# Kernel tuning notes

Hardware: AMD Instinct MI355X
Metric: run time of the kernel (lower is better)

The kernel has to match this reference:

```python
import math
import jax
import jax.numpy as jnp
import numpy as np

SEGMENT_SIZE = 2048   # w (init: segment_size)
DILATION_RATE = 4     # r (init: dilation_rate)
D_MODEL = 1024        # init: d_model


def _sparse_indices(n: int, w: int, r: int, head_idx: int) -> np.ndarray:
    """Static SparsifyIndices: per segment of size w, take tokens offset::r.
    Since r divides w, every segment yields exactly m=w//r indices (no -1 pad).
    Returns flat global token indices, shape (S*m,)."""
    S = n // w
    m = w // r
    off = head_idx % r
    seg_start = np.arange(S, dtype=np.int64)[:, None] * w      # (S,1)
    within = off + r * np.arange(m, dtype=np.int64)[None, :]   # (1,m)
    return (seg_start + within).reshape(-1)


def setup_inputs() -> dict:
    key = jax.random.key(0)
    x = jax.random.normal(key, (4, 8192, D_MODEL), dtype=jnp.float32)
    return {"x": x, "head_idx": 1}


def reference(x, head_idx):
    b, n0, d = x.shape
    w, r = SEGMENT_SIZE, DILATION_RATE
    pad = (-n0) % w
    if pad:
        x = jnp.pad(x, ((0, 0), (0, pad), (0, 0)))
    n = n0 + pad
    idx = _sparse_indices(n, w, r, int(head_idx))  # static, (S*m,)
    S, m = n // w, w // r

    # Gather dilated tokens per segment: (b, S, m, d)
    xg = x[:, idx, :].reshape(b, S, m, d)

    # Softmax attention within each sub-segment (q=k=v=xg)
    scores = jnp.einsum('bsid,bsjd->bsij', xg, xg) / math.sqrt(d)  # (b,S,m,m)
    probs = jax.nn.softmax(scores, axis=-1)
    att = jnp.einsum('bsij,bsjd->bsid', probs, xg).reshape(b, S * m, d)

    # MixOutputs: alpha-weighted scatter-add back to full sequence
    denoms = att.sum(-1)                                       # (b, S*m)
    denom_sums = jnp.zeros((b, n), x.dtype).at[:, idx].add(denoms)
    alphas = denoms / denom_sums[:, idx]                       # (b, S*m)
    out = jnp.zeros((b, n, d), x.dtype).at[:, idx, :].add(att * alphas[..., None])
    return out
```

## Files before the change

### kernel.cpp

```cpp
#include <hip/hip_runtime.h>
#include <hip/hip_bf16.h>


typedef __bf16 bf16_t;
typedef __bf16 bf16x8 __attribute__((ext_vector_type(8)));
typedef float floatx4 __attribute__((ext_vector_type(4)));

#define D_MODEL 1024
#define SEG_W   2048
#define RATE    4
#define M_SUB   512
#define NTOK    8192
#define NSEGT   16
#define XG_ELEMS ((long)NSEGT * M_SUB * D_MODEL)

__device__ __forceinline__ void gload16(const bf16_t* g, bf16_t* l) {
    __builtin_amdgcn_global_load_lds(
        (const __attribute__((address_space(1))) void*)g,
        (__attribute__((address_space(3))) void*)l, 16, 0, 0);
}

#define MFMA16(a, b, c) __builtin_amdgcn_mfma_f32_16x16x32_bf16((a), (b), (c), 0, 0, 0)

__global__ __launch_bounds__(256) void gather_kernel(
    const float* __restrict__ x, const int* __restrict__ hidp,
    bf16_t* __restrict__ xg, bf16_t* __restrict__ xgT)
{
    const int off = ((hidp[0] % RATE) + RATE) % RATE;
    const int bid = blockIdx.x;
    const int seg = bid >> 7;
    const int rem = bid & 127;
    const int it  = rem >> 4;
    const int dt  = rem & 15;
    const int b   = seg >> 2, s = seg & 3;

    __shared__ ushort tile[64][65];

    const int t  = threadIdx.x;
    const int r  = t >> 2;
    const int cq = (t & 3) << 4;

    union U8 { bf16x8 v; ushort u[8]; };

    {
        const int  i   = it * 64 + r;
        const long tok = (long)s * SEG_W + off + 4L * i;
        const float* src = x + ((long)b * NTOK + tok) * D_MODEL + dt * 64 + cq;
        float4 f0 = ((const float4*)src)[0];
        float4 f1 = ((const float4*)src)[1];
        float4 f2 = ((const float4*)src)[2];
        float4 f3 = ((const float4*)src)[3];
        U8 lo, hi;
        lo.v[0]=(bf16_t)f0.x; lo.v[1]=(bf16_t)f0.y; lo.v[2]=(bf16_t)f0.z; lo.v[3]=(bf16_t)f0.w;
        lo.v[4]=(bf16_t)f1.x; lo.v[5]=(bf16_t)f1.y; lo.v[6]=(bf16_t)f1.z; lo.v[7]=(bf16_t)f1.w;
        hi.v[0]=(bf16_t)f2.x; hi.v[1]=(bf16_t)f2.y; hi.v[2]=(bf16_t)f2.z; hi.v[3]=(bf16_t)f2.w;
        hi.v[4]=(bf16_t)f3.x; hi.v[5]=(bf16_t)f3.y; hi.v[6]=(bf16_t)f3.z; hi.v[7]=(bf16_t)f3.w;
        bf16_t* dstg = xg + ((long)seg * M_SUB + i) * D_MODEL + dt * 64 + cq;
        *(bf16x8*)(dstg)     = lo.v;
        *(bf16x8*)(dstg + 8) = hi.v;
        #pragma unroll
        for (int j = 0; j < 8; ++j) { tile[r][cq + j] = lo.u[j]; tile[r][cq + 8 + j] = hi.u[j]; }
    }
    __syncthreads();
    {
        const int dc = r;
        const int iq = cq;
        U8 o0, o1;
        #pragma unroll
        for (int j = 0; j < 8; ++j) { o0.u[j] = tile[iq + j][dc]; o1.u[j] = tile[iq + 8 + j][dc]; }
        bf16_t* dstT = xgT + ((long)seg * D_MODEL + dt * 64 + dc) * M_SUB + it * 64 + iq;
        *(bf16x8*)(dstT)     = o0.v;
        *(bf16x8*)(dstT + 8) = o1.v;
    }
}

__global__ __launch_bounds__(512, 2) void attn_kernel(
    const bf16_t* __restrict__ xg, const bf16_t* __restrict__ xgT,
    const int* __restrict__ hidp, float* __restrict__ out)
{
    const int off  = ((hidp[0] % RATE) + RATE) % RATE;
    const int bid0 = blockIdx.x;
    const int sub  = bid0 >> 3;
    const int seg  = (bid0 & 7) * 2 + (sub >> 4);
    const int band = sub & 15;
    const int b = seg >> 2, s = seg & 3;

    const int tid  = threadIdx.x;
    const int w    = tid >> 6;
    const int lane = tid & 63;
    const int l16  = lane & 15;
    const int quad = lane >> 4;

    __shared__ alignas(16) char arena[133120];
    bf16_t* Kring = (bf16_t*)arena;
    float (*redmax)[32] = (float(*)[32])(arena + 131072);
    float (*redsum)[32] = (float(*)[32])(arena + 132096);
    bf16_t* Pl    = (bf16_t*)arena;
    bf16_t* Vring = (bf16_t*)(arena + 32768);

    const bf16_t* xs = xg + (long)seg * M_SUB * D_MODEL;

    const bf16_t* qr0 = xs + (long)(band * 32 + l16) * D_MODEL + quad * 8;
    const bf16_t* qr1 = qr0 + 16 * D_MODEL;

    const bf16_t* ksrc = xs + (long)(w * 64 + (lane >> 2)) * D_MODEL
                            + (((lane & 3) ^ (lane >> 4)) * 8);
    auto stageK = [&](int buf, int t) {
        bf16_t* dst = Kring + buf * 16384 + (w * 64) * 32;
        const bf16_t* src = ksrc + t * 32;
        #pragma unroll
        for (int j = 0; j < 4; ++j)
            gload16(src + j * 16 * D_MODEL, dst + j * 512);
    };

    const bf16_t* vsrc = xgT + ((long)seg * D_MODEL + w * 64 + (lane >> 2)) * M_SUB
                             + (((lane & 3) ^ (lane >> 4)) * 8);
    auto stageV = [&](int buf, int p, int t) {
        bf16_t* dst = Vring + buf * 16384 + (w * 64) * 32;
        const bf16_t* src = vsrc + (long)p * 512 * M_SUB + t * 32;
        #pragma unroll
        for (int j = 0; j < 4; ++j)
            gload16(src + j * 16 * M_SUB, dst + j * 512);
    };

    const int rsw = (l16 >> 2) & 3;

    floatx4 accS[2][4];
    #pragma unroll
    for (int m = 0; m < 2; ++m)
        #pragma unroll
        for (int n = 0; n < 4; ++n) accS[m][n] = (floatx4){0.f, 0.f, 0.f, 0.f};

    bf16x8 qf[4][2];
    #pragma unroll
    for (int p0 = 0; p0 < 3; ++p0) {
        qf[p0][0] = *(const bf16x8*)(qr0 + p0 * 32);
        qf[p0][1] = *(const bf16x8*)(qr1 + p0 * 32);
        stageK(p0, p0);
    }

    #pragma unroll
    for (int t = 0; t < 32; ++t) {
        if (t <= 29)      asm volatile("s_waitcnt vmcnt(12)" ::: "memory");
        else if (t == 30) asm volatile("s_waitcnt vmcnt(6)"  ::: "memory");
        else              asm volatile("s_waitcnt vmcnt(0)"  ::: "memory");

        const bf16_t* Kb = Kring + (t & 3) * 16384;
        bf16x8 Bf[4];
        #pragma unroll
        for (int n = 0; n < 4; ++n) {
            const int row = w * 64 + n * 16 + l16;
            Bf[n] = *(const bf16x8*)&Kb[row * 32 + ((quad ^ rsw) * 8)];
        }
        if (t <= 28) {
            qf[(t + 3) & 3][0] = *(const bf16x8*)(qr0 + (t + 3) * 32);
            qf[(t + 3) & 3][1] = *(const bf16x8*)(qr1 + (t + 3) * 32);
            stageK((t + 3) & 3, t + 3);
        }
        #pragma unroll
        for (int n = 0; n < 4; ++n) {
            accS[0][n] = MFMA16(qf[t & 3][0], Bf[n], accS[0][n]);
            accS[1][n] = MFMA16(qf[t & 3][1], Bf[n], accS[1][n]);
        }
    }

    #pragma unroll
    for (int m = 0; m < 2; ++m)
        #pragma unroll
        for (int n = 0; n < 4; ++n)
            #pragma unroll
            for (int rg = 0; rg < 4; ++rg) accS[m][n][rg] *= 0.03125f;

    float mx[2][4];
    #pragma unroll
    for (int m = 0; m < 2; ++m)
        #pragma unroll
        for (int rg = 0; rg < 4; ++rg)
            mx[m][rg] = fmaxf(fmaxf(accS[m][0][rg], accS[m][1][rg]),
                              fmaxf(accS[m][2][rg], accS[m][3][rg]));
    #pragma unroll
    for (int d = 1; d < 16; d <<= 1)
        #pragma unroll
        for (int m = 0; m < 2; ++m)
            #pragma unroll
            for (int rg = 0; rg < 4; ++rg)
                mx[m][rg] = fmaxf(mx[m][rg], __shfl_xor(mx[m][rg], d, 64));
    if (l16 == 0) {
        #pragma unroll
        for (int m = 0; m < 2; ++m)
            #pragma unroll
            for (int rg = 0; rg < 4; ++rg)
                redmax[w][m * 16 + quad * 4 + rg] = mx[m][rg];
    }
    __syncthreads();
    float gm[2][4];
    #pragma unroll
    for (int m = 0; m < 2; ++m)
        #pragma unroll
        for (int rg = 0; rg < 4; ++rg) {
            const int row = m * 16 + quad * 4 + rg;
            float g = redmax[0][row];
            #pragma unroll
            for (int ww = 1; ww < 8; ++ww) g = fmaxf(g, redmax[ww][row]);
            gm[m][rg] = g;
        }
    float sm[2][4] = {{0.f,0.f,0.f,0.f},{0.f,0.f,0.f,0.f}};
    #pragma unroll
    for (int m = 0; m < 2; ++m)
        #pragma unroll
        for (int n = 0; n < 4; ++n)
            #pragma unroll
            for (int rg = 0; rg < 4; ++rg) {
                const float e = __expf(accS[m][n][rg] - gm[m][rg]);
                accS[m][n][rg] = e;
                sm[m][rg] += e;
            }
    #pragma unroll
    for (int d = 1; d < 16; d <<= 1)
        #pragma unroll
        for (int m = 0; m < 2; ++m)
            #pragma unroll
            for (int rg = 0; rg < 4; ++rg)
                sm[m][rg] += __shfl_xor(sm[m][rg], d, 64);
    if (l16 == 0) {
        #pragma unroll
        for (int m = 0; m < 2; ++m)
            #pragma unroll
            for (int rg = 0; rg < 4; ++rg)
                redsum[w][m * 16 + quad * 4 + rg] = sm[m][rg];
    }
    __syncthreads();
    float iv[2][4];
    #pragma unroll
    for (int m = 0; m < 2; ++m)
        #pragma unroll
        for (int rg = 0; rg < 4; ++rg) {
            const int row = m * 16 + quad * 4 + rg;
            float tt = redsum[0][row];
            #pragma unroll
            for (int ww = 1; ww < 8; ++ww) tt += redsum[ww][row];
            iv[m][rg] = 1.f / tt;
        }

    stageV(0, 0, 0); stageV(1, 0, 1); stageV(2, 0, 2);

    #pragma unroll
    for (int m = 0; m < 2; ++m)
        #pragma unroll
        for (int rg = 0; rg < 4; ++rg) {
            const int row = m * 16 + quad * 4 + rg;
            const float f = iv[m][rg];
            #pragma unroll
            for (int n = 0; n < 4; ++n) {
                const int col = w * 64 + n * 16 + l16;
                const int sw  = (((col >> 3) ^ (row & 7)) << 3) + (col & 7);
                Pl[row * 512 + sw] = (bf16_t)(accS[m][n][rg] * f);
            }
        }
    asm volatile("s_waitcnt lgkmcnt(0)" ::: "memory");
    __builtin_amdgcn_s_barrier();
    __builtin_amdgcn_sched_barrier(0);

    floatx4 accA[2][4], accB[2][4];
    #pragma unroll
    for (int m = 0; m < 2; ++m)
        #pragma unroll
        for (int n = 0; n < 4; ++n) {
            accA[m][n] = (floatx4){0.f, 0.f, 0.f, 0.f};
            accB[m][n] = (floatx4){0.f, 0.f, 0.f, 0.f};
        }

    auto pv_pass = [&](int p, floatx4 (&acc)[2][4]) {
        #pragma unroll
        for (int t = 0; t < 16; ++t) {
            if (t <= 13)      asm volatile("s_waitcnt vmcnt(8)" ::: "memory");
            else if (t == 14) asm volatile("s_waitcnt vmcnt(4)" ::: "memory");
            else              asm volatile("s_waitcnt vmcnt(0)" ::: "memory");

            const bf16_t* Vb = Vring + (t % 3) * 16384;
            bf16x8 Af[2], Bf[4];
            const int ch = (t * 4 + quad) ^ (l16 & 7);
            #pragma unroll
            for (int m = 0; m < 2; ++m)
                Af[m] = *(const bf16x8*)&Pl[(m * 16 + l16) * 512 + ch * 8];
            #pragma unroll
            for (int n = 0; n < 4; ++n) {
                const int row = w * 64 + n * 16 + l16;
                Bf[n] = *(const bf16x8*)&Vb[row * 32 + ((quad ^ rsw) * 8)];
            }
            #pragma unroll
            for (int m = 0; m < 2; ++m)
                #pragma unroll
                for (int n = 0; n < 4; ++n)
                    acc[m][n] = MFMA16(Af[m], Bf[n], acc[m][n]);
            if (t <= 12) stageV(t % 3, p, t + 3);
        }
    };

    pv_pass(0, accA);
    stageV(0, 1, 0); stageV(1, 1, 1); stageV(2, 1, 2);
    pv_pass(1, accB);

    float* obase = out + (long)b * NTOK * D_MODEL;
    #pragma unroll
    for (int m = 0; m < 2; ++m)
        #pragma unroll
        for (int rg = 0; rg < 4; ++rg) {
            const long tok = (long)s * SEG_W + off + 4L * (band * 32 + m * 16 + quad * 4 + rg);
            float* orow = obase + tok * D_MODEL;
            #pragma unroll
            for (int n = 0; n < 4; ++n) {
                const int d = w * 64 + n * 16 + l16;
                __builtin_nontemporal_store(accA[m][n][rg], orow + d);
                __builtin_nontemporal_store(accB[m][n][rg], orow + 512 + d);
            }
        }

    {
        const floatx4 z = {0.f, 0.f, 0.f, 0.f};
        const int chunk = tid & 255;
        const int half  = tid >> 8;
        #pragma unroll 4
        for (int p = 0; p < 48; ++p) {
            const int t = p * 2 + half;
            const int q = t / 3, e = t % 3;
            const int delta = e + (e >= off ? 1 : 0);
            const long tok = (long)s * SEG_W + 4L * (band * 32 + q) + delta;
            __builtin_nontemporal_store(z, (floatx4*)(obase + tok * D_MODEL + chunk * 4));
        }
    }
}

extern "C" void kernel_launch(void* const* d_in, const int* in_sizes, int n_in,
                              void* d_out, int out_size, void* d_ws, size_t ws_size,
                              hipStream_t stream) {
    const float* x   = (const float*)d_in[0];
    const int*   hid = (const int*)d_in[1];
    float*       out = (float*)d_out;
    bf16_t* xg  = (bf16_t*)d_ws;
    bf16_t* xgT = xg + XG_ELEMS;

    gather_kernel<<<dim3(2048), dim3(256), 0, stream>>>(x, hid, xg, xgT);
    attn_kernel<<<dim3(256), dim3(512), 0, stream>>>(xg, xgT, hid, out);
}
```

Before: 253.4 us.

## Load K/V operands directly to registers and move zero-fill into gather kernel

Drops the LDS staging rings for K and V in the attention kernel. Each wave now loads its MFMA B operands straight from global memory into a 7-slot register ring, with counted vmcnt waits. The two PV passes are merged into one 32-step loop, and P fragments are double-buffered from LDS. The zero-fill of the non-selected output rows moves from the attention kernel's tail into the gather kernel, so it overlaps the gather work. The trade-off is much higher register pressure from the register rings and uncoalesced 16-byte row-strided global loads in place of cooperative LDS staging.

```diff
diff --git a/kernel.cpp b/kernel.cpp
--- a/kernel.cpp
+++ b/kernel.cpp
@@ -14,17 +14,28 @@
 #define NSEGT   16
 #define XG_ELEMS ((long)NSEGT * M_SUB * D_MODEL)
 
-__device__ __forceinline__ void gload16(const bf16_t* g, bf16_t* l) {
-    __builtin_amdgcn_global_load_lds(
-        (const __attribute__((address_space(1))) void*)g,
-        (__attribute__((address_space(3))) void*)l, 16, 0, 0);
+#define MFMA16(a, b, c) __builtin_amdgcn_mfma_f32_16x16x32_bf16((a), (b), (c), 0, 0, 0)
+
+__device__ __forceinline__ void vwait(int n) {
+    switch (n) {
+    case 0:  asm volatile("s_waitcnt vmcnt(0)"  ::: "memory"); break;
+    case 4:  asm volatile("s_waitcnt vmcnt(4)"  ::: "memory"); break;
+    case 6:  asm volatile("s_waitcnt vmcnt(6)"  ::: "memory"); break;
+    case 8:  asm volatile("s_waitcnt vmcnt(8)"  ::: "memory"); break;
+    case 12: asm volatile("s_waitcnt vmcnt(12)" ::: "memory"); break;
+    case 16: asm volatile("s_waitcnt vmcnt(16)" ::: "memory"); break;
+    case 18: asm volatile("s_waitcnt vmcnt(18)" ::: "memory"); break;
+    case 20: asm volatile("s_waitcnt vmcnt(20)" ::: "memory"); break;
+    case 24: asm volatile("s_waitcnt vmcnt(24)" ::: "memory"); break;
+    case 30: asm volatile("s_waitcnt vmcnt(30)" ::: "memory"); break;
+    case 36: asm volatile("s_waitcnt vmcnt(36)" ::: "memory"); break;
+    }
 }
-
-#define MFMA16(a, b, c) __builtin_amdgcn_mfma_f32_16x16x32_bf16((a), (b), (c), 0, 0, 0)
 
 __global__ __launch_bounds__(256) void gather_kernel(
     const float* __restrict__ x, const int* __restrict__ hidp,
-    bf16_t* __restrict__ xg, bf16_t* __restrict__ xgT)
+    bf16_t* __restrict__ xg, bf16_t* __restrict__ xgT,
+    float* __restrict__ out)
 {
     const int off = ((hidp[0] % RATE) + RATE) % RATE;
     const int bid = blockIdx.x;
@@ -72,6 +83,22 @@
         *(bf16x8*)(dstT)     = o0.v;
         *(bf16x8*)(dstT + 8) = o1.v;
     }
+
+    {
+        const floatx4 z = {0.f, 0.f, 0.f, 0.f};
+        const int i2 = r;
+        const int c4 = t & 3;
+        float* obase = out + (long)b * NTOK * D_MODEL + dt * 64;
+        #pragma unroll
+        for (int e = 0; e < 3; ++e) {
+            const int delta = e + (e >= off ? 1 : 0);
+            const long tok = (long)s * SEG_W + 4L * (it * 64 + i2) + delta;
+            floatx4* dst = (floatx4*)(obase + tok * D_MODEL);
+            #pragma unroll
+            for (int c = 0; c < 4; ++c)
+                __builtin_nontemporal_store(z, dst + c4 + 4 * c);
+        }
+    }
 }
 
 __global__ __launch_bounds__(512, 2) void attn_kernel(
@@ -91,76 +118,49 @@
     const int l16  = lane & 15;
     const int quad = lane >> 4;
 
-    __shared__ alignas(16) char arena[133120];
-    bf16_t* Kring = (bf16_t*)arena;
-    float (*redmax)[32] = (float(*)[32])(arena + 131072);
-    float (*redsum)[32] = (float(*)[32])(arena + 132096);
-    bf16_t* Pl    = (bf16_t*)arena;
-    bf16_t* Vring = (bf16_t*)(arena + 32768);
+    __shared__ alignas(16) bf16_t Pl[32 * 512];
+    __shared__ float redmax[8][32];
+    __shared__ float redsum[8][32];
 
     const bf16_t* xs = xg + (long)seg * M_SUB * D_MODEL;
 
     const bf16_t* qr0 = xs + (long)(band * 32 + l16) * D_MODEL + quad * 8;
     const bf16_t* qr1 = qr0 + 16 * D_MODEL;
-
-    const bf16_t* ksrc = xs + (long)(w * 64 + (lane >> 2)) * D_MODEL
-                            + (((lane & 3) ^ (lane >> 4)) * 8);
-    auto stageK = [&](int buf, int t) {
-        bf16_t* dst = Kring + buf * 16384 + (w * 64) * 32;
-        const bf16_t* src = ksrc + t * 32;
-        #pragma unroll
-        for (int j = 0; j < 4; ++j)
-            gload16(src + j * 16 * D_MODEL, dst + j * 512);
+    const bf16_t* kb0 = xs + (long)(w * 64 + l16) * D_MODEL + quad * 8;
+    const bf16_t* kb1 = kb0 + 16 * D_MODEL;
+    const bf16_t* kb2 = kb0 + 32 * D_MODEL;
+    const bf16_t* kb3 = kb0 + 48 * D_MODEL;
+
+    floatx4 accS[2][4];
+    #pragma unroll
+    for (int m = 0; m < 2; ++m)
+        #pragma unroll
+        for (int n = 0; n < 4; ++n) accS[m][n] = (floatx4){0.f, 0.f, 0.f, 0.f};
+
+    bf16x8 qf[7][2], kf[7][4];
+    auto issueQK = [&](int slot, int tt) {
+        const int o = tt * 32;
+        qf[slot][0] = *(const bf16x8*)(qr0 + o);
+        qf[slot][1] = *(const bf16x8*)(qr1 + o);
+        kf[slot][0] = *(const bf16x8*)(kb0 + o);
+        kf[slot][1] = *(const bf16x8*)(kb1 + o);
+        kf[slot][2] = *(const bf16x8*)(kb2 + o);
+        kf[slot][3] = *(const bf16x8*)(kb3 + o);
     };
 
-    const bf16_t* vsrc = xgT + ((long)seg * D_MODEL + w * 64 + (lane >> 2)) * M_SUB
-                             + (((lane & 3) ^ (lane >> 4)) * 8);
-    auto stageV = [&](int buf, int p, int t) {
-        bf16_t* dst = Vring + buf * 16384 + (w * 64) * 32;
-        const bf16_t* src = vsrc + (long)p * 512 * M_SUB + t * 32;
-        #pragma unroll
-        for (int j = 0; j < 4; ++j)
-            gload16(src + j * 16 * M_SUB, dst + j * 512);
-    };
-
-    const int rsw = (l16 >> 2) & 3;
-
-    floatx4 accS[2][4];
-    #pragma unroll
-    for (int m = 0; m < 2; ++m)
-        #pragma unroll
-        for (int n = 0; n < 4; ++n) accS[m][n] = (floatx4){0.f, 0.f, 0.f, 0.f};
-
-    bf16x8 qf[4][2];
-    #pragma unroll
-    for (int p0 = 0; p0 < 3; ++p0) {
-        qf[p0][0] = *(const bf16x8*)(qr0 + p0 * 32);
-        qf[p0][1] = *(const bf16x8*)(qr1 + p0 * 32);
-        stageK(p0, p0);
-    }
+    #pragma unroll
+    for (int p = 0; p < 6; ++p) issueQK(p, p);
 
     #pragma unroll
     for (int t = 0; t < 32; ++t) {
-        if (t <= 29)      asm volatile("s_waitcnt vmcnt(12)" ::: "memory");
-        else if (t == 30) asm volatile("s_waitcnt vmcnt(6)"  ::: "memory");
-        else              asm volatile("s_waitcnt vmcnt(0)"  ::: "memory");
-
-        const bf16_t* Kb = Kring + (t & 3) * 16384;
-        bf16x8 Bf[4];
+        if (t + 6 < 32) issueQK((t + 6) % 7, t + 6);
+        const int ahead = (31 - t) < 6 ? (31 - t) : 6;
+        vwait(6 * ahead);
+        const int sl = t % 7;
         #pragma unroll
         for (int n = 0; n < 4; ++n) {
-            const int row = w * 64 + n * 16 + l16;
-            Bf[n] = *(const bf16x8*)&Kb[row * 32 + ((quad ^ rsw) * 8)];
-        }
-        if (t <= 28) {
-            qf[(t + 3) & 3][0] = *(const bf16x8*)(qr0 + (t + 3) * 32);
-            qf[(t + 3) & 3][1] = *(const bf16x8*)(qr1 + (t + 3) * 32);
-            stageK((t + 3) & 3, t + 3);
-        }
-        #pragma unroll
-        for (int n = 0; n < 4; ++n) {
-            accS[0][n] = MFMA16(qf[t & 3][0], Bf[n], accS[0][n]);
-            accS[1][n] = MFMA16(qf[t & 3][1], Bf[n], accS[1][n]);
+            accS[0][n] = MFMA16(qf[sl][0], kf[sl][n], accS[0][n]);
+            accS[1][n] = MFMA16(qf[sl][1], kf[sl][n], accS[1][n]);
         }
     }
 
@@ -242,7 +242,22 @@
             iv[m][rg] = 1.f / tt;
         }
 
-    stageV(0, 0, 0); stageV(1, 0, 1); stageV(2, 0, 2);
+    const bf16_t* vb0 = xgT + ((long)seg * D_MODEL + w * 64 + l16) * M_SUB + quad * 8;
+    const bf16_t* vb1 = vb0 + 16 * M_SUB;
+    const bf16_t* vb2 = vb0 + 32 * M_SUB;
+    const bf16_t* vb3 = vb0 + 48 * M_SUB;
+
+    bf16x8 vf[7][4];
+    auto issueV = [&](int slot, int t) {
+        const int tt = t & 15;
+        const long po = (long)(t >> 4) * 512 * M_SUB + tt * 32;
+        vf[slot][0] = *(const bf16x8*)(vb0 + po);
+        vf[slot][1] = *(const bf16x8*)(vb1 + po);
+        vf[slot][2] = *(const bf16x8*)(vb2 + po);
+        vf[slot][3] = *(const bf16x8*)(vb3 + po);
+    };
+    #pragma unroll
+    for (int p = 0; p < 6; ++p) issueV(p, p);
 
     #pragma unroll
     for (int m = 0; m < 2; ++m)
@@ -270,36 +285,36 @@
             accB[m][n] = (floatx4){0.f, 0.f, 0.f, 0.f};
         }
 
-    auto pv_pass = [&](int p, floatx4 (&acc)[2][4]) {
-        #pragma unroll
-        for (int t = 0; t < 16; ++t) {
-            if (t <= 13)      asm volatile("s_waitcnt vmcnt(8)" ::: "memory");
-            else if (t == 14) asm volatile("s_waitcnt vmcnt(4)" ::: "memory");
-            else              asm volatile("s_waitcnt vmcnt(0)" ::: "memory");
-
-            const bf16_t* Vb = Vring + (t % 3) * 16384;
-            bf16x8 Af[2], Bf[4];
-            const int ch = (t * 4 + quad) ^ (l16 & 7);
-            #pragma unroll
-            for (int m = 0; m < 2; ++m)
-                Af[m] = *(const bf16x8*)&Pl[(m * 16 + l16) * 512 + ch * 8];
+    bf16x8 pf[2][2];
+    auto loadP = [&](int slot, int t) {
+        const int tt = t & 15;
+        const int ch = (tt * 4 + quad) ^ (l16 & 7);
+        pf[slot][0] = *(const bf16x8*)&Pl[(l16) * 512 + ch * 8];
+        pf[slot][1] = *(const bf16x8*)&Pl[(16 + l16) * 512 + ch * 8];
+    };
+    loadP(0, 0);
+
+    #pragma unroll
+    for (int t = 0; t < 32; ++t) {
+        if (t + 6 < 32) issueV((t + 6) % 7, t + 6);
+        const int ahead = (31 - t) < 6 ? (31 - t) : 6;
+        vwait(4 * ahead);
+        if (t + 1 < 32) loadP((t + 1) & 1, t + 1);
+        const int sl = t % 7;
+        if (t < 16) {
             #pragma unroll
             for (int n = 0; n < 4; ++n) {
-                const int row = w * 64 + n * 16 + l16;
-                Bf[n] = *(const bf16x8*)&Vb[row * 32 + ((quad ^ rsw) * 8)];
-            }
-            #pragma unroll
-            for (int m = 0; m < 2; ++m)
-                #pragma unroll
-                for (int n = 0; n < 4; ++n)
-                    acc[m][n] = MFMA16(Af[m], Bf[n], acc[m][n]);
-            if (t <= 12) stageV(t % 3, p, t + 3);
-        }
-    };
-
-    pv_pass(0, accA);
-    stageV(0, 1, 0); stageV(1, 1, 1); stageV(2, 1, 2);
-    pv_pass(1, accB);
+                accA[0][n] = MFMA16(pf[t & 1][0], vf[sl][n], accA[0][n]);
+                accA[1][n] = MFMA16(pf[t & 1][1], vf[sl][n], accA[1][n]);
+            }
+        } else {
+            #pragma unroll
+            for (int n = 0; n < 4; ++n) {
+                accB[0][n] = MFMA16(pf[t & 1][0], vf[sl][n], accB[0][n]);
+                accB[1][n] = MFMA16(pf[t & 1][1], vf[sl][n], accB[1][n]);
+            }
+        }
+    }
 
     float* obase = out + (long)b * NTOK * D_MODEL;
     #pragma unroll
@@ -315,20 +330,6 @@
                 __builtin_nontemporal_store(accB[m][n][rg], orow + 512 + d);
             }
         }
-
-    {
-        const floatx4 z = {0.f, 0.f, 0.f, 0.f};
-        const int chunk = tid & 255;
-        const int half  = tid >> 8;
-        #pragma unroll 4
-        for (int p = 0; p < 48; ++p) {
-            const int t = p * 2 + half;
-            const int q = t / 3, e = t % 3;
-            const int delta = e + (e >= off ? 1 : 0);
-            const long tok = (long)s * SEG_W + 4L * (band * 32 + q) + delta;
-            __builtin_nontemporal_store(z, (floatx4*)(obase + tok * D_MODEL + chunk * 4));
-        }
-    }
 }
 
 extern "C" void kernel_launch(void* const* d_in, const int* in_sizes, int n_in,
@@ -340,6 +341,6 @@
     bf16_t* xg  = (bf16_t*)d_ws;
     bf16_t* xgT = xg + XG_ELEMS;
 
-    gather_kernel<<<dim3(2048), dim3(256), 0, stream>>>(x, hid, xg, xgT);
+    gather_kernel<<<dim3(2048), dim3(256), 0, stream>>>(x, hid, xg, xgT, out);
     attn_kernel<<<dim3(256), dim3(512), 0, stream>>>(xg, xgT, hid, out);
 }
```

After: 298.1 us. 1.18x slower.

## Split fused attention into QK-softmax and PV kernels; move zero-fill into gather

Applied to the files above, without the earlier changes.

Splits the single attention kernel in two. The first computes QK^T and the softmax and writes normalized probabilities P to global memory. The second streams P and V through one continuous 32-step pipelined loop that covers both output halves, instead of two separate passes that each restart the pipeline. Zeroing the non-selected output rows moves from the attention kernel to the gather kernel. This smooths the PV pipeline and frees LDS, at the cost of an extra kernel launch and a global round trip for P (16x512x512 bf16 values).

```diff
diff --git a/kernel.cpp b/kernel.cpp
--- a/kernel.cpp
+++ b/kernel.cpp
@@ -13,6 +13,7 @@
 #define NTOK    8192
 #define NSEGT   16
 #define XG_ELEMS ((long)NSEGT * M_SUB * D_MODEL)
+#define P_ELEMS  ((long)NSEGT * M_SUB * M_SUB)
 
 __device__ __forceinline__ void gload16(const bf16_t* g, bf16_t* l) {
     __builtin_amdgcn_global_load_lds(
@@ -22,9 +23,18 @@
 
 #define MFMA16(a, b, c) __builtin_amdgcn_mfma_f32_16x16x32_bf16((a), (b), (c), 0, 0, 0)
 
+__device__ __forceinline__ void vwait(int n) {
+    switch (n) {
+    case 0:  asm volatile("s_waitcnt vmcnt(0)"  ::: "memory"); break;
+    case 6:  asm volatile("s_waitcnt vmcnt(6)"  ::: "memory"); break;
+    case 12: asm volatile("s_waitcnt vmcnt(12)" ::: "memory"); break;
+    }
+}
+
 __global__ __launch_bounds__(256) void gather_kernel(
     const float* __restrict__ x, const int* __restrict__ hidp,
-    bf16_t* __restrict__ xg, bf16_t* __restrict__ xgT)
+    bf16_t* __restrict__ xg, bf16_t* __restrict__ xgT,
+    float* __restrict__ out)
 {
     const int off = ((hidp[0] % RATE) + RATE) % RATE;
     const int bid = blockIdx.x;
@@ -72,10 +82,208 @@
         *(bf16x8*)(dstT)     = o0.v;
         *(bf16x8*)(dstT + 8) = o1.v;
     }
-}
-
-__global__ __launch_bounds__(512, 2) void attn_kernel(
-    const bf16_t* __restrict__ xg, const bf16_t* __restrict__ xgT,
+
+    {
+        const floatx4 z = {0.f, 0.f, 0.f, 0.f};
+        #pragma unroll
+        for (int k = 0; k < 12; ++k) {
+            const int z0 = bid * 12 + k;
+            const int zseg = z0 / 1536;
+            const int zz   = z0 - zseg * 1536;
+            const int i    = zz / 3;
+            const int e    = zz - 3 * i;
+            const int delta = e + (e >= off ? 1 : 0);
+            const int zb = zseg >> 2, zs = zseg & 3;
+            const long tok = (long)zs * SEG_W + 4L * i + delta;
+            float* dst = out + ((long)zb * NTOK + tok) * D_MODEL + t * 4;
+            __builtin_nontemporal_store(z, (floatx4*)dst);
+        }
+    }
+}
+
+__global__ __launch_bounds__(512, 2) void qk_kernel(
+    const bf16_t* __restrict__ xg, bf16_t* __restrict__ Pg)
+{
+    const int bid0 = blockIdx.x;
+    const int sub  = bid0 >> 3;
+    const int seg  = (bid0 & 7) * 2 + (sub >> 4);
+    const int band = sub & 15;
+
+    const int tid  = threadIdx.x;
+    const int w    = tid >> 6;
+    const int lane = tid & 63;
+    const int l16  = lane & 15;
+    const int quad = lane >> 4;
+
+    __shared__ alignas(16) char arena[133120];
+    bf16_t* Kring = (bf16_t*)arena;
+    float (*redmax)[32] = (float(*)[32])(arena + 131072);
+    float (*redsum)[32] = (float(*)[32])(arena + 132096);
+    bf16_t* Pl = (bf16_t*)arena;
+
+    const bf16_t* xs = xg + (long)seg * M_SUB * D_MODEL;
+
+    const bf16_t* qr0 = xs + (long)(band * 32 + l16) * D_MODEL + quad * 8;
+    const bf16_t* qr1 = qr0 + 16 * D_MODEL;
+    const bf16_t* ksrc = xs + (long)(w * 64 + (lane >> 2)) * D_MODEL
+                            + (((lane & 3) ^ (lane >> 4)) * 8);
+    auto stageK = [&](int buf, int t) {
+        bf16_t* dst = Kring + buf * 16384 + (w * 64) * 32;
+        const bf16_t* src = ksrc + t * 32;
+        #pragma unroll
+        for (int j = 0; j < 4; ++j)
+            gload16(src + j * 16 * D_MODEL, dst + j * 512);
+    };
+
+    const int rsw = (l16 >> 2) & 3;
+
+    floatx4 accS[2][4];
+    #pragma unroll
+    for (int m = 0; m < 2; ++m)
+        #pragma unroll
+        for (int n = 0; n < 4; ++n) accS[m][n] = (floatx4){0.f, 0.f, 0.f, 0.f};
+
+    bf16x8 qf[4][2];
+    #pragma unroll
+    for (int p0 = 0; p0 < 3; ++p0) {
+        qf[p0][0] = *(const bf16x8*)(qr0 + p0 * 32);
+        qf[p0][1] = *(const bf16x8*)(qr1 + p0 * 32);
+        stageK(p0, p0);
+    }
+
+    #pragma unroll
+    for (int t = 0; t < 32; ++t) {
+        if (t <= 29)      vwait(12);
+        else if (t == 30) vwait(6);
+        else              vwait(0);
+
+        const bf16_t* Kb = Kring + (t & 3) * 16384;
+        bf16x8 Bf[4];
+        #pragma unroll
+        for (int n = 0; n < 4; ++n) {
+            const int row = w * 64 + n * 16 + l16;
+            Bf[n] = *(const bf16x8*)&Kb[row * 32 + ((quad ^ rsw) * 8)];
+        }
+        if (t <= 28) {
+            qf[(t + 3) & 3][0] = *(const bf16x8*)(qr0 + (t + 3) * 32);
+            qf[(t + 3) & 3][1] = *(const bf16x8*)(qr1 + (t + 3) * 32);
+            stageK((t + 3) & 3, t + 3);
+        }
+        #pragma unroll
+        for (int n = 0; n < 4; ++n) {
+            accS[0][n] = MFMA16(qf[t & 3][0], Bf[n], accS[0][n]);
+            accS[1][n] = MFMA16(qf[t & 3][1], Bf[n], accS[1][n]);
+        }
+    }
+
+    #pragma unroll
+    for (int m = 0; m < 2; ++m)
+        #pragma unroll
+        for (int n = 0; n < 4; ++n)
+            #pragma unroll
+            for (int rg = 0; rg < 4; ++rg) accS[m][n][rg] *= 0.03125f;
+
+    float mx[2][4];
+    #pragma unroll
+    for (int m = 0; m < 2; ++m)
+        #pragma unroll
+        for (int rg = 0; rg < 4; ++rg)
+            mx[m][rg] = fmaxf(fmaxf(accS[m][0][rg], accS[m][1][rg]),
+                              fmaxf(accS[m][2][rg], accS[m][3][rg]));
+    #pragma unroll
+    for (int d = 1; d < 16; d <<= 1)
+        #pragma unroll
+        for (int m = 0; m < 2; ++m)
+            #pragma unroll
+            for (int rg = 0; rg < 4; ++rg)
+                mx[m][rg] = fmaxf(mx[m][rg], __shfl_xor(mx[m][rg], d, 64));
+    if (l16 == 0) {
+        #pragma unroll
+        for (int m = 0; m < 2; ++m)
+            #pragma unroll
+            for (int rg = 0; rg < 4; ++rg)
+                redmax[w][m * 16 + quad * 4 + rg] = mx[m][rg];
+    }
+    __syncthreads();
+    float gm[2][4];
+    #pragma unroll
+    for (int m = 0; m < 2; ++m)
+        #pragma unroll
+        for (int rg = 0; rg < 4; ++rg) {
+            const int row = m * 16 + quad * 4 + rg;
+            float g = redmax[0][row];
+            #pragma unroll
+            for (int ww = 1; ww < 8; ++ww) g = fmaxf(g, redmax[ww][row]);
+            gm[m][rg] = g;
+        }
+    float sm[2][4] = {{0.f,0.f,0.f,0.f},{0.f,0.f,0.f,0.f}};
+    #pragma unroll
+    for (int m = 0; m < 2; ++m)
+        #pragma unroll
+        for (int n = 0; n < 4; ++n)
+            #pragma unroll
+            for (int rg = 0; rg < 4; ++rg) {
+                const float e = __expf(accS[m][n][rg] - gm[m][rg]);
+                accS[m][n][rg] = e;
+                sm[m][rg] += e;
+            }
+    #pragma unroll
+    for (int d = 1; d < 16; d <<= 1)
+        #pragma unroll
+        for (int m = 0; m < 2; ++m)
+            #pragma unroll
+            for (int rg = 0; rg < 4; ++rg)
+                sm[m][rg] += __shfl_xor(sm[m][rg], d, 64);
+    if (l16 == 0) {
+        #pragma unroll
+        for (int m = 0; m < 2; ++m)
+            #pragma unroll
+            for (int rg = 0; rg < 4; ++rg)
+                redsum[w][m * 16 + quad * 4 + rg] = sm[m][rg];
+    }
+    __syncthreads();
+    float iv[2][4];
+    #pragma unroll
+    for (int m = 0; m < 2; ++m)
+        #pragma unroll
+        for (int rg = 0; rg < 4; ++rg) {
+            const int row = m * 16 + quad * 4 + rg;
+            float tt = redsum[0][row];
+            #pragma unroll
+            for (int ww = 1; ww < 8; ++ww) tt += redsum[ww][row];
+            iv[m][rg] = 1.f / tt;
+        }
+
+    #pragma unroll
+    for (int m = 0; m < 2; ++m)
+        #pragma unroll
+        for (int rg = 0; rg < 4; ++rg) {
+            const int row = m * 16 + quad * 4 + rg;
+            const float f = iv[m][rg];
+            #pragma unroll
+            for (int n = 0; n < 4; ++n) {
+                const int col = w * 64 + n * 16 + l16;
+                const int sw  = (((col >> 3) ^ (row & 7)) << 3) + (col & 7);
+                Pl[row * 512 + sw] = (bf16_t)(accS[m][n][rg] * f);
+            }
+        }
+    __syncthreads();
+
+    {
+        const int prow = tid >> 4;
+        const int pc0  = tid & 15;
+        bf16_t* pd = Pg + (long)seg * M_SUB * M_SUB + (long)(band * 32 + prow) * M_SUB;
+        #pragma unroll
+        for (int j = 0; j < 4; ++j) {
+            const int c = pc0 + 16 * j;
+            bf16x8 v = *(const bf16x8*)&Pl[prow * 512 + ((c ^ (prow & 7)) * 8)];
+            *(bf16x8*)&pd[c * 8] = v;
+        }
+    }
+}
+
+__global__ __launch_bounds__(512, 2) void pv_kernel(
+    const bf16_t* __restrict__ Pg, const bf16_t* __restrict__ xgT,
     const int* __restrict__ hidp, float* __restrict__ out)
 {
     const int off  = ((hidp[0] % RATE) + RATE) % RATE;
@@ -91,175 +299,23 @@
     const int l16  = lane & 15;
     const int quad = lane >> 4;
 
-    __shared__ alignas(16) char arena[133120];
-    bf16_t* Kring = (bf16_t*)arena;
-    float (*redmax)[32] = (float(*)[32])(arena + 131072);
-    float (*redsum)[32] = (float(*)[32])(arena + 132096);
-    bf16_t* Pl    = (bf16_t*)arena;
-    bf16_t* Vring = (bf16_t*)(arena + 32768);
-
-    const bf16_t* xs = xg + (long)seg * M_SUB * D_MODEL;
-
-    const bf16_t* qr0 = xs + (long)(band * 32 + l16) * D_MODEL + quad * 8;
-    const bf16_t* qr1 = qr0 + 16 * D_MODEL;
-
-    const bf16_t* ksrc = xs + (long)(w * 64 + (lane >> 2)) * D_MODEL
-                            + (((lane & 3) ^ (lane >> 4)) * 8);
-    auto stageK = [&](int buf, int t) {
-        bf16_t* dst = Kring + buf * 16384 + (w * 64) * 32;
-        const bf16_t* src = ksrc + t * 32;
-        #pragma unroll
-        for (int j = 0; j < 4; ++j)
-            gload16(src + j * 16 * D_MODEL, dst + j * 512);
-    };
+    __shared__ alignas(16) bf16_t Vring[4 * 16384];
 
     const bf16_t* vsrc = xgT + ((long)seg * D_MODEL + w * 64 + (lane >> 2)) * M_SUB
                              + (((lane & 3) ^ (lane >> 4)) * 8);
-    auto stageV = [&](int buf, int p, int t) {
+    auto stageV = [&](int buf, int t) {
         bf16_t* dst = Vring + buf * 16384 + (w * 64) * 32;
-        const bf16_t* src = vsrc + (long)p * 512 * M_SUB + t * 32;
+        const bf16_t* src = vsrc + (long)(t >> 4) * 512 * M_SUB + (t & 15) * 32;
         #pragma unroll
         for (int j = 0; j < 4; ++j)
             gload16(src + j * 16 * M_SUB, dst + j * 512);
     };
 
+    const bf16_t* pr0 = Pg + (long)seg * M_SUB * M_SUB
+                           + (long)(band * 32 + l16) * M_SUB + quad * 8;
+    const bf16_t* pr1 = pr0 + 16 * M_SUB;
+
     const int rsw = (l16 >> 2) & 3;
-
-    floatx4 accS[2][4];
-    #pragma unroll
-    for (int m = 0; m < 2; ++m)
-        #pragma unroll
-        for (int n = 0; n < 4; ++n) accS[m][n] = (floatx4){0.f, 0.f, 0.f, 0.f};
-
-    bf16x8 qf[4][2];
-    #pragma unroll
-    for (int p0 = 0; p0 < 3; ++p0) {
-        qf[p0][0] = *(const bf16x8*)(qr0 + p0 * 32);
-        qf[p0][1] = *(const bf16x8*)(qr1 + p0 * 32);
-        stageK(p0, p0);
-    }
-
-    #pragma unroll
-    for (int t = 0; t < 32; ++t) {
-        if (t <= 29)      asm volatile("s_waitcnt vmcnt(12)" ::: "memory");
-        else if (t == 30) asm volatile("s_waitcnt vmcnt(6)"  ::: "memory");
-        else              asm volatile("s_waitcnt vmcnt(0)"  ::: "memory");
-
-        const bf16_t* Kb = Kring + (t & 3) * 16384;
-        bf16x8 Bf[4];
-        #pragma unroll
-        for (int n = 0; n < 4; ++n) {
-            const int row = w * 64 + n * 16 + l16;
-            Bf[n] = *(const bf16x8*)&Kb[row * 32 + ((quad ^ rsw) * 8)];
-        }
-        if (t <= 28) {
-            qf[(t + 3) & 3][0] = *(const bf16x8*)(qr0 + (t + 3) * 32);
-            qf[(t + 3) & 3][1] = *(const bf16x8*)(qr1 + (t + 3) * 32);
-            stageK((t + 3) & 3, t + 3);
-        }
-        #pragma unroll
-        for (int n = 0; n < 4; ++n) {
-            accS[0][n] = MFMA16(qf[t & 3][0], Bf[n], accS[0][n]);
-            accS[1][n] = MFMA16(qf[t & 3][1], Bf[n], accS[1][n]);
-        }
-    }
-
-    #pragma unroll
-    for (int m = 0; m < 2; ++m)
-        #pragma unroll
-        for (int n = 0; n < 4; ++n)
-            #pragma unroll
-            for (int rg = 0; rg < 4; ++rg) accS[m][n][rg] *= 0.03125f;
-
-    float mx[2][4];
-    #pragma unroll
-    for (int m = 0; m < 2; ++m)
-        #pragma unroll
-        for (int rg = 0; rg < 4; ++rg)
-            mx[m][rg] = fmaxf(fmaxf(accS[m][0][rg], accS[m][1][rg]),
-                              fmaxf(accS[m][2][rg], accS[m][3][rg]));
-    #pragma unroll
-    for (int d = 1; d < 16; d <<= 1)
-        #pragma unroll
-        for (int m = 0; m < 2; ++m)
-            #pragma unroll
-            for (int rg = 0; rg < 4; ++rg)
-                mx[m][rg] = fmaxf(mx[m][rg], __shfl_xor(mx[m][rg], d, 64));
-    if (l16 == 0) {
-        #pragma unroll
-        for (int m = 0; m < 2; ++m)
-            #pragma unroll
-            for (int rg = 0; rg < 4; ++rg)
-                redmax[w][m * 16 + quad * 4 + rg] = mx[m][rg];
-    }
-    __syncthreads();
-    float gm[2][4];
-    #pragma unroll
-    for (int m = 0; m < 2; ++m)
-        #pragma unroll
-        for (int rg = 0; rg < 4; ++rg) {
-            const int row = m * 16 + quad * 4 + rg;
-            float g = redmax[0][row];
-            #pragma unroll
-            for (int ww = 1; ww < 8; ++ww) g = fmaxf(g, redmax[ww][row]);
-            gm[m][rg] = g;
-        }
-    float sm[2][4] = {{0.f,0.f,0.f,0.f},{0.f,0.f,0.f,0.f}};
-    #pragma unroll
-    for (int m = 0; m < 2; ++m)
-        #pragma unroll
-        for (int n = 0; n < 4; ++n)
-            #pragma unroll
-            for (int rg = 0; rg < 4; ++rg) {
-                const float e = __expf(accS[m][n][rg] - gm[m][rg]);
-                accS[m][n][rg] = e;
-                sm[m][rg] += e;
-            }
-    #pragma unroll
-    for (int d = 1; d < 16; d <<= 1)
-        #pragma unroll
-        for (int m = 0; m < 2; ++m)
-            #pragma unroll
-            for (int rg = 0; rg < 4; ++rg)
-                sm[m][rg] += __shfl_xor(sm[m][rg], d, 64);
-    if (l16 == 0) {
-        #pragma unroll
-        for (int m = 0; m < 2; ++m)
-            #pragma unroll
-            for (int rg = 0; rg < 4; ++rg)
-                redsum[w][m * 16 + quad * 4 + rg] = sm[m][rg];
-    }
-    __syncthreads();
-    float iv[2][4];
-    #pragma unroll
-    for (int m = 0; m < 2; ++m)
-        #pragma unroll
-        for (int rg = 0; rg < 4; ++rg) {
-            const int row = m * 16 + quad * 4 + rg;
-            float tt = redsum[0][row];
-            #pragma unroll
-            for (int ww = 1; ww < 8; ++ww) tt += redsum[ww][row];
-            iv[m][rg] = 1.f / tt;
-        }
-
-    stageV(0, 0, 0); stageV(1, 0, 1); stageV(2, 0, 2);
-
-    #pragma unroll
-    for (int m = 0; m < 2; ++m)
-        #pragma unroll
-        for (int rg = 0; rg < 4; ++rg) {
-            const int row = m * 16 + quad * 4 + rg;
-            const float f = iv[m][rg];
-            #pragma unroll
-            for (int n = 0; n < 4; ++n) {
-                const int col = w * 64 + n * 16 + l16;
-                const int sw  = (((col >> 3) ^ (row & 7)) << 3) + (col & 7);
-                Pl[row * 512 + sw] = (bf16_t)(accS[m][n][rg] * f);
-            }
-        }
-    asm volatile("s_waitcnt lgkmcnt(0)" ::: "memory");
-    __builtin_amdgcn_s_barrier();
-    __builtin_amdgcn_sched_barrier(0);
 
     floatx4 accA[2][4], accB[2][4];
     #pragma unroll
@@ -270,36 +326,46 @@
             accB[m][n] = (floatx4){0.f, 0.f, 0.f, 0.f};
         }
 
-    auto pv_pass = [&](int p, floatx4 (&acc)[2][4]) {
-        #pragma unroll
-        for (int t = 0; t < 16; ++t) {
-            if (t <= 13)      asm volatile("s_waitcnt vmcnt(8)" ::: "memory");
-            else if (t == 14) asm volatile("s_waitcnt vmcnt(4)" ::: "memory");
-            else              asm volatile("s_waitcnt vmcnt(0)" ::: "memory");
-
-            const bf16_t* Vb = Vring + (t % 3) * 16384;
-            bf16x8 Af[2], Bf[4];
-            const int ch = (t * 4 + quad) ^ (l16 & 7);
-            #pragma unroll
-            for (int m = 0; m < 2; ++m)
-                Af[m] = *(const bf16x8*)&Pl[(m * 16 + l16) * 512 + ch * 8];
+    bf16x8 pf[4][2];
+    #pragma unroll
+    for (int p0 = 0; p0 < 3; ++p0) {
+        pf[p0][0] = *(const bf16x8*)(pr0 + (p0 & 15) * 32);
+        pf[p0][1] = *(const bf16x8*)(pr1 + (p0 & 15) * 32);
+        stageV(p0, p0);
+    }
+
+    #pragma unroll
+    for (int t = 0; t < 32; ++t) {
+        if (t <= 29)      vwait(12);
+        else if (t == 30) vwait(6);
+        else              vwait(0);
+
+        const bf16_t* Vb = Vring + (t & 3) * 16384;
+        bf16x8 Bf[4];
+        #pragma unroll
+        for (int n = 0; n < 4; ++n) {
+            const int row = w * 64 + n * 16 + l16;
+            Bf[n] = *(const bf16x8*)&Vb[row * 32 + ((quad ^ rsw) * 8)];
+        }
+        if (t <= 28) {
+            pf[(t + 3) & 3][0] = *(const bf16x8*)(pr0 + ((t + 3) & 15) * 32);
+            pf[(t + 3) & 3][1] = *(const bf16x8*)(pr1 + ((t + 3) & 15) * 32);
+            stageV((t + 3) & 3, t + 3);
+        }
+        if (t < 16) {
             #pragma unroll
             for (int n = 0; n < 4; ++n) {
-                const int row = w * 64 + n * 16 + l16;
-                Bf[n] = *(const bf16x8*)&Vb[row * 32 + ((quad ^ rsw) * 8)];
-            }
-            #pragma unroll
-            for (int m = 0; m < 2; ++m)
-                #pragma unroll
-                for (int n = 0; n < 4; ++n)
-                    acc[m][n] = MFMA16(Af[m], Bf[n], acc[m][n]);
-            if (t <= 12) stageV(t % 3, p, t + 3);
-        }
-    };
-
-    pv_pass(0, accA);
-    stageV(0, 1, 0); stageV(1, 1, 1); stageV(2, 1, 2);
-    pv_pass(1, accB);
+                accA[0][n] = MFMA16(pf[t & 3][0], Bf[n], accA[0][n]);
+                accA[1][n] = MFMA16(pf[t & 3][1], Bf[n], accA[1][n]);
+            }
+        } else {
+            #pragma unroll
+            for (int n = 0; n < 4; ++n) {
+                accB[0][n] = MFMA16(pf[t & 3][0], Bf[n], accB[0][n]);
+                accB[1][n] = MFMA16(pf[t & 3][1], Bf[n], accB[1][n]);
+            }
+        }
+    }
 
     float* obase = out + (long)b * NTOK * D_MODEL;
     #pragma unroll
@@ -315,20 +381,6 @@
                 __builtin_nontemporal_store(accB[m][n][rg], orow + 512 + d);
             }
         }
-
-    {
-        const floatx4 z = {0.f, 0.f, 0.f, 0.f};
-        const int chunk = tid & 255;
-        const int half  = tid >> 8;
-        #pragma unroll 4
-        for (int p = 0; p < 48; ++p) {
-            const int t = p * 2 + half;
-            const int q = t / 3, e = t % 3;
-            const int delta = e + (e >= off ? 1 : 0);
-            const long tok = (long)s * SEG_W + 4L * (band * 32 + q) + delta;
-            __builtin_nontemporal_store(z, (floatx4*)(obase + tok * D_MODEL + chunk * 4));
-        }
-    }
 }
 
 extern "C" void kernel_launch(void* const* d_in, const int* in_sizes, int n_in,
@@ -339,7 +391,9 @@
     float*       out = (float*)d_out;
     bf16_t* xg  = (bf16_t*)d_ws;
     bf16_t* xgT = xg + XG_ELEMS;
-
-    gather_kernel<<<dim3(2048), dim3(256), 0, stream>>>(x, hid, xg, xgT);
-    attn_kernel<<<dim3(256), dim3(512), 0, stream>>>(xg, xgT, hid, out);
-}
+    bf16_t* Pg  = xgT + XG_ELEMS;
+
+    gather_kernel<<<dim3(2048), dim3(256), 0, stream>>>(x, hid, xg, xgT, out);
+    qk_kernel<<<dim3(256), dim3(512), 0, stream>>>(xg, Pg);
+    pv_kernel<<<dim3(256), dim3(512), 0, stream>>>(Pg, xgT, hid, out);
+}
```

Measured after the change: 269.7 us. 1.06x slower.

## Merge PV passes into one pipelined loop and interleave zero-fill stores

Applied to the files above, without the earlier changes.

Fuses the two 16-step PV passes into a single 32-step loop with a continuous 3-buffer V prefetch ring, so there is no pipeline drain and refill between the two output halves. The zero-fill stores for non-selected tokens are spread across the PV loop iterations instead of running after the epilogue, so they overlap with MFMA work. It also raises wave priority around the MFMA blocks with s_setprio. The vmcnt wait counts are hand-tuned to count both loads and the interleaved stores, so an error there could leave LDS data unready.

```diff
diff --git a/kernel.cpp b/kernel.cpp
--- a/kernel.cpp
+++ b/kernel.cpp
@@ -21,6 +21,18 @@
 }
 
 #define MFMA16(a, b, c) __builtin_amdgcn_mfma_f32_16x16x32_bf16((a), (b), (c), 0, 0, 0)
+
+__device__ __forceinline__ void vwait(int n) {
+    switch (n) {
+    case 0:  asm volatile("s_waitcnt vmcnt(0)"  ::: "memory"); break;
+    case 4:  asm volatile("s_waitcnt vmcnt(4)"  ::: "memory"); break;
+    case 6:  asm volatile("s_waitcnt vmcnt(6)"  ::: "memory"); break;
+    case 8:  asm volatile("s_waitcnt vmcnt(8)"  ::: "memory"); break;
+    case 10: asm volatile("s_waitcnt vmcnt(10)" ::: "memory"); break;
+    case 12: asm volatile("s_waitcnt vmcnt(12)" ::: "memory"); break;
+    case 14: asm volatile("s_waitcnt vmcnt(14)" ::: "memory"); break;
+    }
+}
 
 __global__ __launch_bounds__(256) void gather_kernel(
     const float* __restrict__ x, const int* __restrict__ hidp,
@@ -99,6 +111,7 @@
     bf16_t* Vring = (bf16_t*)(arena + 32768);
 
     const bf16_t* xs = xg + (long)seg * M_SUB * D_MODEL;
+    float* obase = out + (long)b * NTOK * D_MODEL;
 
     const bf16_t* qr0 = xs + (long)(band * 32 + l16) * D_MODEL + quad * 8;
     const bf16_t* qr1 = qr0 + 16 * D_MODEL;
@@ -115,12 +128,24 @@
 
     const bf16_t* vsrc = xgT + ((long)seg * D_MODEL + w * 64 + (lane >> 2)) * M_SUB
                              + (((lane & 3) ^ (lane >> 4)) * 8);
-    auto stageV = [&](int buf, int p, int t) {
+    auto stageV = [&](int buf, int t) {
         bf16_t* dst = Vring + buf * 16384 + (w * 64) * 32;
-        const bf16_t* src = vsrc + (long)p * 512 * M_SUB + t * 32;
+        const bf16_t* src = vsrc + (long)(t >> 4) * 512 * M_SUB + (t & 15) * 32;
         #pragma unroll
         for (int j = 0; j < 4; ++j)
             gload16(src + j * 16 * M_SUB, dst + j * 512);
+    };
+
+    auto zstore = [&](int t) {
+        const floatx4 z = {0.f, 0.f, 0.f, 0.f};
+        const int r2 = tid >> 7;
+        const int j  = t * 4 + r2;
+        const int q  = j / 3, e = j - 3 * (j / 3);
+        const int delta = e + (e >= off ? 1 : 0);
+        const long tok = (long)s * SEG_W + 4L * (band * 32 + q) + delta;
+        float* dst = obase + tok * D_MODEL + (tid & 127) * 4;
+        __builtin_nontemporal_store(z, (floatx4*)dst);
+        __builtin_nontemporal_store(z, (floatx4*)(dst + 512));
     };
 
     const int rsw = (l16 >> 2) & 3;
@@ -141,9 +166,9 @@
 
     #pragma unroll
     for (int t = 0; t < 32; ++t) {
-        if (t <= 29)      asm volatile("s_waitcnt vmcnt(12)" ::: "memory");
-        else if (t == 30) asm volatile("s_waitcnt vmcnt(6)"  ::: "memory");
-        else              asm volatile("s_waitcnt vmcnt(0)"  ::: "memory");
+        if (t <= 29)      vwait(12);
+        else if (t == 30) vwait(6);
+        else              vwait(0);
 
         const bf16_t* Kb = Kring + (t & 3) * 16384;
         bf16x8 Bf[4];
@@ -157,11 +182,13 @@
             qf[(t + 3) & 3][1] = *(const bf16x8*)(qr1 + (t + 3) * 32);
             stageK((t + 3) & 3, t + 3);
         }
+        __builtin_amdgcn_s_setprio(1);
         #pragma unroll
         for (int n = 0; n < 4; ++n) {
             accS[0][n] = MFMA16(qf[t & 3][0], Bf[n], accS[0][n]);
             accS[1][n] = MFMA16(qf[t & 3][1], Bf[n], accS[1][n]);
         }
+        __builtin_amdgcn_s_setprio(0);
     }
 
     #pragma unroll
@@ -242,7 +269,7 @@
             iv[m][rg] = 1.f / tt;
         }
 
-    stageV(0, 0, 0); stageV(1, 0, 1); stageV(2, 0, 2);
+    stageV(0, 0); stageV(1, 1); stageV(2, 2);
 
     #pragma unroll
     for (int m = 0; m < 2; ++m)
@@ -270,38 +297,50 @@
             accB[m][n] = (floatx4){0.f, 0.f, 0.f, 0.f};
         }
 
-    auto pv_pass = [&](int p, floatx4 (&acc)[2][4]) {
-        #pragma unroll
-        for (int t = 0; t < 16; ++t) {
-            if (t <= 13)      asm volatile("s_waitcnt vmcnt(8)" ::: "memory");
-            else if (t == 14) asm volatile("s_waitcnt vmcnt(4)" ::: "memory");
-            else              asm volatile("s_waitcnt vmcnt(0)" ::: "memory");
-
-            const bf16_t* Vb = Vring + (t % 3) * 16384;
-            bf16x8 Af[2], Bf[4];
-            const int ch = (t * 4 + quad) ^ (l16 & 7);
-            #pragma unroll
-            for (int m = 0; m < 2; ++m)
-                Af[m] = *(const bf16x8*)&Pl[(m * 16 + l16) * 512 + ch * 8];
+    #pragma unroll
+    for (int t = 0; t < 32; ++t) {
+        if      (t == 0)  vwait(8);
+        else if (t == 1)  vwait(10);
+        else if (t == 2)  vwait(12);
+        else if (t <= 24) vwait(14);
+        else if (t == 25) vwait(12);
+        else if (t == 26) vwait(10);
+        else if (t <= 29) vwait(8);
+        else if (t == 30) vwait(4);
+        else              vwait(0);
+
+        const bf16_t* Vb = Vring + (t % 3) * 16384;
+        bf16x8 Af[2], Bf[4];
+        const int ch = ((t & 15) * 4 + quad) ^ (l16 & 7);
+        #pragma unroll
+        for (int m = 0; m < 2; ++m)
+            Af[m] = *(const bf16x8*)&Pl[(m * 16 + l16) * 512 + ch * 8];
+        #pragma unroll
+        for (int n = 0; n < 4; ++n) {
+            const int row = w * 64 + n * 16 + l16;
+            Bf[n] = *(const bf16x8*)&Vb[row * 32 + ((quad ^ rsw) * 8)];
+        }
+        __builtin_amdgcn_s_setprio(1);
+        if (t < 16) {
             #pragma unroll
             for (int n = 0; n < 4; ++n) {
-                const int row = w * 64 + n * 16 + l16;
-                Bf[n] = *(const bf16x8*)&Vb[row * 32 + ((quad ^ rsw) * 8)];
-            }
-            #pragma unroll
-            for (int m = 0; m < 2; ++m)
-                #pragma unroll
-                for (int n = 0; n < 4; ++n)
-                    acc[m][n] = MFMA16(Af[m], Bf[n], acc[m][n]);
-            if (t <= 12) stageV(t % 3, p, t + 3);
-        }
-    };
-
-    pv_pass(0, accA);
-    stageV(0, 1, 0); stageV(1, 1, 1); stageV(2, 1, 2);
-    pv_pass(1, accB);
-
-    float* obase = out + (long)b * NTOK * D_MODEL;
+                accA[0][n] = MFMA16(Af[0], Bf[n], accA[0][n]);
+                accA[1][n] = MFMA16(Af[1], Bf[n], accA[1][n]);
+            }
+        } else {
+            #pragma unroll
+            for (int n = 0; n < 4; ++n) {
+                accB[0][n] = MFMA16(Af[0], Bf[n], accB[0][n]);
+                accB[1][n] = MFMA16(Af[1], Bf[n], accB[1][n]);
+            }
+        }
+        __builtin_amdgcn_s_setprio(0);
+        __builtin_amdgcn_sched_barrier(0);
+        if (t <= 28) stageV((t + 3) % 3, t + 3);
+        __builtin_amdgcn_sched_barrier(0);
+        if (t <= 23) zstore(t);
+    }
+
     #pragma unroll
     for (int m = 0; m < 2; ++m)
         #pragma unroll
@@ -315,20 +354,6 @@
                 __builtin_nontemporal_store(accB[m][n][rg], orow + 512 + d);
             }
         }
-
-    {
-        const floatx4 z = {0.f, 0.f, 0.f, 0.f};
-        const int chunk = tid & 255;
-        const int half  = tid >> 8;
-        #pragma unroll 4
-        for (int p = 0; p < 48; ++p) {
-            const int t = p * 2 + half;
-            const int q = t / 3, e = t % 3;
-            const int delta = e + (e >= off ? 1 : 0);
-            const long tok = (long)s * SEG_W + 4L * (band * 32 + q) + delta;
-            __builtin_nontemporal_store(z, (floatx4*)(obase + tok * D_MODEL + chunk * 4));
-        }
-    }
 }
 
 extern "C" void kernel_launch(void* const* d_in, const int* in_sizes, int n_in,
```

After: 243.0 us. 4.1% less time.
